# Optimization experiments

Measured on AMD Instinct MI355X. Metric: run time of the kernel, lower is better.

The kernel has to match this reference:

```python
import jax, jax.numpy as jnp
import numpy as np

N_NODES = 100000
N_EDGES = 1_600_000


def _glorot(key, shape):
    fan_in, fan_out = shape
    s = jnp.sqrt(6.0 / (fan_in + fan_out)).astype(jnp.float32)
    return jax.random.uniform(key, shape, jnp.float32, -1.0, 1.0) * s


def setup_inputs() -> dict:
    key = jax.random.key(0)
    ks = jax.random.split(key, 6)
    x = jax.random.normal(ks[0], (N_NODES, 88), jnp.float32)
    edge_index = jax.random.randint(ks[1], (2, N_EDGES), 0, N_NODES, dtype=jnp.int32)
    return {
        "x": x,
        "W1": _glorot(ks[2], (88, 65)), "b1": jnp.zeros((65,), jnp.float32),
        "W2": _glorot(ks[3], (65, 50)), "b2": jnp.zeros((50,), jnp.float32),
        "W3": _glorot(ks[4], (50, 65)), "b3": jnp.zeros((65,), jnp.float32),
        "W4": _glorot(ks[5], (65, 88)), "b4": jnp.zeros((88,), jnp.float32),
        "edge_index": edge_index,
    }


def _gcn_conv(h, W, b, src, dst, norm, n):
    # PyG GCNConv: transform, then normalized neighbor aggregation (self-loops
    # already folded into src/dst/norm).
    h = h @ W                                  # [N, out]
    msg = h[src] * norm[:, None]               # [E+N, out] gather
    return jax.ops.segment_sum(msg, dst, num_segments=n) + b  # scatter-add


def reference(x, W1, b1, W2, b2, W3, b3, W4, b4, edge_index):
    n = x.shape[0]
    loop = jnp.arange(n, dtype=edge_index.dtype)
    src = jnp.concatenate([edge_index[0], loop])   # add self-loops
    dst = jnp.concatenate([edge_index[1], loop])
    deg = jax.ops.segment_sum(jnp.ones_like(dst, dtype=x.dtype), dst, num_segments=n)
    dinv = jnp.where(deg > 0, jax.lax.rsqrt(deg), 0.0)
    norm = dinv[src] * dinv[dst]                   # D^-1/2 (A+I) D^-1/2 edge weights

    # encoder
    h = jax.nn.relu(_gcn_conv(x, W1, b1, src, dst, norm, n))
    h = _gcn_conv(h, W2, b2, src, dst, norm, n)
    # decoder
    h = jax.nn.relu(_gcn_conv(h, W3, b3, src, dst, norm, n))
    return _gcn_conv(h, W4, b4, src, dst, norm, n)
```

## Files before the change

### kernel.cpp

```cpp
#include <hip/hip_runtime.h>

#define BS 256
#define FB 1024
#define NB 256
#define CHUNK 4096
#define CAP 64
#define LCAP 8192
#define GRID_F 1024

using half8 = __attribute__((ext_vector_type(8))) _Float16;

template<typename T>
__device__ __forceinline__ void load8f(const T* p, float (&d)[8]) {
    if constexpr (sizeof(T) == 4) {
        float4 a = *(const float4*)p;
        float4 b = *(const float4*)(p + 4);
        d[0] = a.x; d[1] = a.y; d[2] = a.z; d[3] = a.w;
        d[4] = b.x; d[5] = b.y; d[6] = b.z; d[7] = b.w;
    } else {
        half8 v = *(const half8*)p;
        #pragma unroll
        for (int j = 0; j < 8; ++j) d[j] = (float)v[j];
    }
}
template<typename T>
__device__ __forceinline__ void store8f(T* p, const float (&d)[8]) {
    if constexpr (sizeof(T) == 4) {
        *(float4*)p       = make_float4(d[0], d[1], d[2], d[3]);
        *(float4*)(p + 4) = make_float4(d[4], d[5], d[6], d[7]);
    } else {
        half8 h;
        #pragma unroll
        for (int j = 0; j < 8; ++j) h[j] = (_Float16)d[j];
        *(half8*)p = h;
    }
}


__global__ __launch_bounds__(BS) void k_bucket_g1(
        const int* __restrict__ src, const int* __restrict__ dst,
        unsigned* __restrict__ bbuf, int* __restrict__ bcounts,
        int E, unsigned long long invB, int bsz, int nch,
        const float* __restrict__ x, const float* __restrict__ W1,
        _Float16* __restrict__ hA, int N) {
    constexpr int K = 88, M = 65, LDIN = 88, LDOUT = 72;
    constexpr int CG = 9;
    constexpr int WSTR = K * 8 + 4;
    __shared__ float sh[CG * WSTR];

    if ((int)blockIdx.x < nch) {
        int* lcnt = (int*)sh;
        for (int t = threadIdx.x; t < NB; t += BS) lcnt[t] = 0;
        __syncthreads();
        int base_e = blockIdx.x * CHUNK;
        unsigned* mybuf = bbuf + (size_t)blockIdx.x * NB * CAP;
        #pragma unroll
        for (int j = 0; j < CHUNK / BS; ++j) {
            int e = base_e + j * BS + threadIdx.x;
            if (e < E) {
                int d = dst[e];
                int s = src[e];
                int b = (int)(((unsigned long long)(unsigned)d * invB) >> 40);
                int doff = d - b * bsz;
                int pos = atomicAdd(&lcnt[b], 1);
                if (pos < CAP)
                    mybuf[b * CAP + pos] = ((unsigned)doff << 17) | (unsigned)s;
            }
        }
        __syncthreads();
        for (int t = threadIdx.x; t < NB; t += BS)
            bcounts[blockIdx.x * NB + t] = min(lcnt[t], CAP);
        return;
    }

    float* Wl = sh;
    for (int idx = threadIdx.x; idx < CG * WSTR; idx += BS) {
        int cg = idx / WSTR, rem = idx - cg * WSTR;
        int k = rem >> 3, j = rem & 7;
        int m = cg * 8 + j;
        Wl[idx] = (rem < K * 8 && m < M) ? W1[(size_t)k * M + m] : 0.f;
    }
    __syncthreads();

    int bid = blockIdx.x - nch;
    int nrq = (N + 3) >> 2;
    int idx = bid * BS + threadIdx.x;
    if (idx >= nrq * CG) return;
    int rq = idx / CG;
    int cg = idx - rq * CG;
    int c0 = cg * 8;
    int r0 = rq * 4;
    const float* wb = &Wl[cg * WSTR];

    const float* h[4];
    #pragma unroll
    for (int r = 0; r < 4; ++r) {
        int rr = r0 + r; rr = (rr < N) ? rr : (N - 1);
        h[r] = x + (size_t)rr * LDIN;
    }
    float acc[4][8];
    #pragma unroll
    for (int r = 0; r < 4; ++r)
        #pragma unroll
        for (int m = 0; m < 8; ++m) acc[r][m] = 0.f;

    #pragma unroll 2
    for (int k = 0; k < K; k += 8) {
        float p[4][8];
        load8f(h[0] + k, p[0]);
        load8f(h[1] + k, p[1]);
        load8f(h[2] + k, p[2]);
        load8f(h[3] + k, p[3]);
        const float* wl = wb + k * 8;
        #pragma unroll
        for (int j = 0; j < 8; ++j) {
            float4 wa = *(const float4*)(wl + j * 8);
            float4 wc = *(const float4*)(wl + j * 8 + 4);
            const float wv[8] = {wa.x, wa.y, wa.z, wa.w, wc.x, wc.y, wc.z, wc.w};
            #pragma unroll
            for (int r = 0; r < 4; ++r)
                #pragma unroll
                for (int m = 0; m < 8; ++m)
                    acc[r][m] = fmaf(p[r][j], wv[m], acc[r][m]);
        }
    }
    #pragma unroll
    for (int r = 0; r < 4; ++r) {
        int rr = r0 + r;
        if (rr >= N) break;
        float v[8];
        #pragma unroll
        for (int m = 0; m < 8; ++m) {
            int c = c0 + m;
            v[m] = (c < M) ? acc[r][m] : 0.f;
        }
        store8f(hA + (size_t)rr * LDOUT + c0, v);
    }
}

__global__ __launch_bounds__(FB) void k_cnt(const unsigned* __restrict__ bbuf, const int* __restrict__ bcounts,
                                            int* __restrict__ cnt, int nch, int bsz, int N) {
    __shared__ int lhist[512];
    for (int t = threadIdx.x; t < 512; t += FB) lhist[t] = 0;
    __syncthreads();
    int b = blockIdx.x;
    int lo = b * bsz;
    int total = nch * CAP;
    for (int idx = threadIdx.x; idx < total; idx += FB) {
        int seg = idx >> 6, slot = idx & 63;
        int c = bcounts[seg * NB + b];
        if (slot < c)
            atomicAdd(&lhist[bbuf[((size_t)seg * NB + b) * CAP + slot] >> 17], 1);
    }
    __syncthreads();
    int hi = min(N, lo + bsz);
    for (int t = threadIdx.x; t < hi - lo; t += FB) cnt[lo + t] = lhist[t];
}

__global__ __launch_bounds__(BS) void k_scan1(const int* __restrict__ cnt, int* __restrict__ bsum,
                                              float* __restrict__ dinv, int N) {
    __shared__ int s[BS];
    int i = blockIdx.x * BS + threadIdx.x;
    int v = (i < N) ? cnt[i] : 0;
    if (i < N) dinv[i] = rsqrtf((float)(v + 1));
    s[threadIdx.x] = v;
    __syncthreads();
    for (int off = BS / 2; off > 0; off >>= 1) {
        if (threadIdx.x < off) s[threadIdx.x] += s[threadIdx.x + off];
        __syncthreads();
    }
    if (threadIdx.x == 0) bsum[blockIdx.x] = s[0];
}

__global__ __launch_bounds__(512) void k_scan2(int* bsum, int nb) {
    __shared__ int s[512];
    int t = threadIdx.x;
    int v = (t < nb) ? bsum[t] : 0;
    s[t] = v;
    __syncthreads();
    for (int off = 1; off < 512; off <<= 1) {
        int u = (t >= off) ? s[t - off] : 0;
        __syncthreads();
        s[t] += u;
        __syncthreads();
    }
    if (t < nb) bsum[t] = s[t] - v;
}

__global__ __launch_bounds__(BS) void k_scan3(const int* __restrict__ cnt, const int* __restrict__ boff,
                                              int* __restrict__ row_ptr, int N) {
    __shared__ int s[BS];
    int t = threadIdx.x;
    int i = blockIdx.x * BS + t;
    int v = (i < N) ? cnt[i] : 0;
    s[t] = v;
    __syncthreads();
    for (int off = 1; off < BS; off <<= 1) {
        int u = (t >= off) ? s[t - off] : 0;
        __syncthreads();
        s[t] += u;
        __syncthreads();
    }
    int base = boff[blockIdx.x];
    if (i < N) row_ptr[i] = base + s[t] - v;
    if (i == N - 1) row_ptr[N] = base + s[t];
}

__global__ __launch_bounds__(FB) void k_fill2(const unsigned* __restrict__ bbuf, const int* __restrict__ bcounts,
                                              const int* __restrict__ row_ptr, const float* __restrict__ dinv,
                                              uint2* __restrict__ entries,
                                              int nch, int bsz, int N) {
    __shared__ int cur[512];
    __shared__ float ldinv[512];
    __shared__ unsigned sorted[LCAP];

    int b = blockIdx.x;
    int lo = b * bsz;
    int hi = min(N, lo + bsz);
    int gbase = row_ptr[lo];
    int tot = row_ptr[hi] - gbase;
    for (int t = threadIdx.x; t < hi - lo; t += FB) {
        cur[t] = row_ptr[lo + t] - gbase;
        ldinv[t] = dinv[lo + t];
    }
    __syncthreads();

    int total = nch * CAP;
    for (int idx = threadIdx.x; idx < total; idx += FB) {
        int seg = idx >> 6, slot = idx & 63;
        int c = bcounts[seg * NB + b];
        if (slot < c) {
            unsigned u = bbuf[((size_t)seg * NB + b) * CAP + slot];
            int p = atomicAdd(&cur[u >> 17], 1);
            if (p < LCAP) sorted[p] = u;
        }
    }
    __syncthreads();

    for (int t = threadIdx.x; t < tot; t += FB) {
        unsigned u = sorted[t];
        int s = (int)(u & 0x1FFFFu);
        int doff = (int)(u >> 17);
        float w = dinv[s] * ldinv[doff];
        entries[gbase + t] = make_uint2((unsigned)s, __float_as_uint(w));
    }
}

template<typename TIN, typename TOUT, int M, int M8, int LDI, int LDO, bool BIAS, bool RELU>
__global__ __launch_bounds__(BS) void k_agg(const TIN* __restrict__ T, TOUT* __restrict__ out,
                                            const int* __restrict__ row_ptr, const uint2* __restrict__ entries,
                                            const float* __restrict__ dinv, const float* __restrict__ bias,
                                            int N) {
    constexpr int CG = M8 / 8;
    int idx = blockIdx.x * BS + threadIdx.x;
    if (idx >= N * CG) return;
    int i  = idx / CG;
    int cg = idx - i * CG;
    int c0 = cg * 8;

    float di = dinv[i];
    float w0 = di * di;
    float t0[8];
    load8f(T + (size_t)i * LDI + c0, t0);
    float a0[8], a1[8];
    #pragma unroll
    for (int m = 0; m < 8; ++m) { a0[m] = w0 * t0[m]; a1[m] = 0.f; }

    int e0 = row_ptr[i], e1 = row_ptr[i + 1];
    for (int e = e0; e < e1; e += 8) {
        unsigned sidx[8];
        float w[8];
        #pragma unroll
        for (int j = 0; j < 8; ++j) {
            int ee = e + j;
            int ec = (ee < e1) ? ee : (e1 - 1);
            uint2 u = entries[ec];
            sidx[j] = u.x;
            w[j] = (ee < e1) ? __uint_as_float(u.y) : 0.f;
        }
        #pragma unroll
        for (int j = 0; j < 8; ++j) {
            float g[8];
            load8f(T + (size_t)sidx[j] * LDI + c0, g);
            if (j & 1) {
                #pragma unroll
                for (int m = 0; m < 8; ++m) a1[m] = fmaf(w[j], g[m], a1[m]);
            } else {
                #pragma unroll
                for (int m = 0; m < 8; ++m) a0[m] = fmaf(w[j], g[m], a0[m]);
            }
        }
    }

    #pragma unroll
    for (int m = 0; m < 8; ++m) {
        float v = a0[m] + a1[m];
        if (BIAS && (c0 + m) < M) v += bias[c0 + m];
        if (RELU) v = fmaxf(v, 0.f);
        a0[m] = v;
    }
    store8f(out + (size_t)i * LDO + c0, a0);
}

template<typename TIN, typename TOUT,
         int MA, int MA8, int LDI,
         int MG, int MG8, int LDO,
         int RPB,
         bool ABIAS, bool ARELU, bool GBIAS, bool GRELU>
__global__ __launch_bounds__(BS) void k_agg_gemm(
        const TIN* __restrict__ T, TOUT* __restrict__ out,
        const int* __restrict__ row_ptr, const uint2* __restrict__ entries,
        const float* __restrict__ dinv, const float* __restrict__ Wg,
        const float* __restrict__ ab, const float* __restrict__ gb, int N) {
    static_assert(sizeof(TIN) == 2, "fused kernel expects f16 input rows");
    constexpr int CGA = MA8 / 8;
    constexpr int CGG = MG8 / 8;
    constexpr int K = MA;
    constexpr int WSTR = K * 8 + 4;
    constexpr int BC = 32;

    __shared__ float Wl[CGG * WSTR];
    __shared__ float srow[2][RPB][MA8];

    for (int idx = threadIdx.x; idx < CGG * WSTR; idx += BS) {
        int cg = idx / WSTR, rem = idx - cg * WSTR;
        int k = rem >> 3, j = rem & 7;
        int m = cg * 8 + j;
        Wl[idx] = (rem < K * 8 && m < MG) ? Wg[(size_t)k * MG + m] : 0.f;
    }

    const int t = threadIdx.x;
    const int rA = t / CGA, cgA = t - rA * CGA, c0A = cgA * 8;
    const bool hasA = (rA < RPB);
    const int rB = t / CGG, cgB = t - rB * CGG, c0B = cgB * 8;
    const bool hasB = (rB < RPB);
    const float* wbB = &Wl[cgB * WSTR];
    const int ntiles = (N + RPB - 1) / RPB;

    for (int s = 0; ; ++s) {
        int tA = (int)blockIdx.x + s * (int)gridDim.x;
        int tB = (int)blockIdx.x + (s - 1) * (int)gridDim.x;
        bool anyA = (tA < ntiles);
        bool anyB = (s >= 1) && (tB < ntiles);
        if (!anyA && !anyB) break;
        int bufA = s & 1, bufB = bufA ^ 1;

        int iA = tA * RPB + rA;
        bool doA = anyA && hasA && (iA < N);
        int iB = tB * RPB + rB;
        bool doB = anyB && hasB && (iB < N);

        float bacc[8];
        #pragma unroll
        for (int m = 0; m < 8; ++m) bacc[m] = 0.f;
        int bk = 0;
        const float* hrow = &srow[bufB][hasB ? rB : 0][0];

        if (doA) {
            float di = dinv[iA];
            float w0 = di * di;
            float t0[8];
            load8f(T + (size_t)iA * LDI + c0A, t0);
            float a0[8], a1[8];
            #pragma unroll
            for (int m = 0; m < 8; ++m) { a0[m] = w0 * t0[m]; a1[m] = 0.f; }

            int e0 = row_ptr[iA], e1 = row_ptr[iA + 1];
            for (int e = e0; e < e1; e += 8) {
                unsigned sidx[8];
                float w[8];
                #pragma unroll
                for (int j = 0; j < 8; ++j) {
                    int ee = e + j;
                    int ec = (ee < e1) ? ee : (e1 - 1);
                    uint2 u = entries[ec];
                    sidx[j] = u.x;
                    w[j] = (ee < e1) ? __uint_as_float(u.y) : 0.f;
                }
                half8 g[8];
                #pragma unroll
                for (int j = 0; j < 8; ++j)
                    g[j] = *(const half8*)(T + (size_t)sidx[j] * LDI + c0A);
                if (doB) {
                    int lim = bk + BC; if (lim > K) lim = K;
                    for (; bk < lim; ++bk) {
                        float hv = hrow[bk];
                        const float* wl = wbB + bk * 8;
                        float4 wa = *(const float4*)wl;
                        float4 wc = *(const float4*)(wl + 4);
                        bacc[0] = fmaf(hv, wa.x, bacc[0]);
                        bacc[1] = fmaf(hv, wa.y, bacc[1]);
                        bacc[2] = fmaf(hv, wa.z, bacc[2]);
                        bacc[3] = fmaf(hv, wa.w, bacc[3]);
                        bacc[4] = fmaf(hv, wc.x, bacc[4]);
                        bacc[5] = fmaf(hv, wc.y, bacc[5]);
                        bacc[6] = fmaf(hv, wc.z, bacc[6]);
                        bacc[7] = fmaf(hv, wc.w, bacc[7]);
                    }
                }
                #pragma unroll
                for (int j = 0; j < 8; ++j) {
                    if (j & 1) {
                        #pragma unroll
                        for (int m = 0; m < 8; ++m) a1[m] = fmaf(w[j], (float)g[j][m], a1[m]);
                    } else {
                        #pragma unroll
                        for (int m = 0; m < 8; ++m) a0[m] = fmaf(w[j], (float)g[j][m], a0[m]);
                    }
                }
            }
            #pragma unroll
            for (int m = 0; m < 8; ++m) {
                float v = a0[m] + a1[m];
                if (ABIAS && (c0A + m) < MA) v += ab[c0A + m];
                if (ARELU) v = fmaxf(v, 0.f);
                srow[bufA][rA][c0A + m] = v;
            }
        }
        if (doB) {
            for (; bk < K; ++bk) {
                float hv = hrow[bk];
                const float* wl = wbB + bk * 8;
                float4 wa = *(const float4*)wl;
                float4 wc = *(const float4*)(wl + 4);
                bacc[0] = fmaf(hv, wa.x, bacc[0]);
                bacc[1] = fmaf(hv, wa.y, bacc[1]);
                bacc[2] = fmaf(hv, wa.z, bacc[2]);
                bacc[3] = fmaf(hv, wa.w, bacc[3]);
                bacc[4] = fmaf(hv, wc.x, bacc[4]);
                bacc[5] = fmaf(hv, wc.y, bacc[5]);
                bacc[6] = fmaf(hv, wc.z, bacc[6]);
                bacc[7] = fmaf(hv, wc.w, bacc[7]);
            }
            float v[8];
            #pragma unroll
            for (int m = 0; m < 8; ++m) {
                int c = c0B + m;
                bool in = (c < MG);
                float xv = in ? bacc[m] : 0.f;
                if (GBIAS && in) xv += gb[c];
                if (GRELU) xv = fmaxf(xv, 0.f);
                v[m] = xv;
            }
            store8f(out + (size_t)iB * LDO + c0B, v);
        }
        __syncthreads();
    }
}


extern "C" void kernel_launch(void* const* d_in, const int* in_sizes, int n_in,
                              void* d_out, int out_size, void* d_ws, size_t ws_size,
                              hipStream_t stream) {
    const float* x  = (const float*)d_in[0];
    const float* W1 = (const float*)d_in[1];
    const float* b1 = (const float*)d_in[2];
    const float* W2 = (const float*)d_in[3];
    const float* b2 = (const float*)d_in[4];
    const float* W3 = (const float*)d_in[5];
    const float* b3 = (const float*)d_in[6];
    const float* W4 = (const float*)d_in[7];
    const float* b4 = (const float*)d_in[8];
    const int* edge_index = (const int*)d_in[9];

    const int N = in_sizes[0] / 88;
    const int E = in_sizes[9] / 2;
    const int* src = edge_index;
    const int* dst = edge_index + E;

    const int nch = (E + CHUNK - 1) / CHUNK;
    const int bsz = (N + NB - 1) / NB;
    const unsigned long long invB = ((1ull << 40) + bsz - 1) / bsz;

    auto al = [](size_t b) { return (b + 255) & ~(size_t)255; };
    char* p = (char*)d_ws;
    auto carve = [&](size_t bytes) { void* r = p; p += (bytes + 255) & ~(size_t)255; return r; };
    int*   cnt     = (int*)  carve((size_t)N * 4);
    float* dinv    = (float*)carve((size_t)N * 4);
    int*   row_ptr = (int*)  carve((size_t)(N + 1) * 4);
    int*   bsum    = (int*)  carve(4096);
    uint2* entries = (uint2*)carve((size_t)E * 8);
    _Float16* hA   = (_Float16*)carve((size_t)N * 72 * 2);

    char* ub = p;
    int*      bcounts = (int*)ub;
    unsigned* bbuf    = (unsigned*)(ub + al((size_t)nch * NB * 4));
    size_t csr_bytes  = al((size_t)nch * NB * 4) + al((size_t)nch * NB * CAP * 4);

    size_t hbytes = al((size_t)N * 72 * 2);
    _Float16* hC = (_Float16*)ub;
    _Float16* hD = (_Float16*)(ub + hbytes);
    size_t h_bytes_tot = 2 * hbytes;

    p = ub + (csr_bytes > h_bytes_tot ? csr_bytes : h_bytes_tot);
    (void)p; (void)ws_size;

    int gN = (N + BS - 1) / BS;
    int g1b = (((N + 3) / 4) * 9 + BS - 1) / BS;

    k_bucket_g1<<<nch + g1b, BS, 0, stream>>>(src, dst, bbuf, bcounts, E, invB, bsz, nch,
                                              x, W1, hA, N);
    k_cnt   <<<NB, FB, 0, stream>>>(bbuf, bcounts, cnt, nch, bsz, N);
    k_scan1 <<<gN, BS, 0, stream>>>(cnt, bsum, dinv, N);
    k_scan2 <<<1, 512, 0, stream>>>(bsum, gN);
    k_scan3 <<<gN, BS, 0, stream>>>(cnt, bsum, row_ptr, N);
    k_fill2 <<<NB, FB, 0, stream>>>(bbuf, bcounts, row_ptr, dinv, entries, nch, bsz, N);

    auto agg_grid = [&](int CG) { return (N * CG + BS - 1) / BS; };

    k_agg_gemm<_Float16, _Float16, 65, 72, 72, 50, 56, 56, 28, true, true, false, false>
        <<<GRID_F, BS, 0, stream>>>(hA, hC, row_ptr, entries, dinv, W2, b1, nullptr, N);
    k_agg<_Float16, _Float16, 50, 56, 56, 56, true, false>
        <<<agg_grid(7), BS, 0, stream>>>(hC, hD, row_ptr, entries, dinv, b2, N);
    k_agg_gemm<_Float16, _Float16, 50, 56, 56, 65, 72, 72, 28, false, false, true, true>
        <<<GRID_F, BS, 0, stream>>>(hD, hA, row_ptr, entries, dinv, W3, nullptr, b3, N);
    k_agg_gemm<_Float16, float, 65, 72, 72, 88, 88, 88, 23, false, false, true, false>
        <<<GRID_F, BS, 0, stream>>>(hA, (float*)d_out, row_ptr, entries, dinv, W4, nullptr, b4, N);
}
```

Before: 422.8 us.

## Split fused agg-gemm block into dedicated gather and GEMM warp roles

The fused aggregation+GEMM kernel now runs gather and GEMM in separate warps. The first three waves (192 threads) do the sparse neighbour gather for tile s, and the last wave computes the dense GEMM for tile s-1 out of shared memory. Before, every thread interleaved both jobs. Rows per block and grid sizes are retuned so the gather role fits in 192 threads. The gain is warp specialisation with less register pressure per path, at the cost of a single GEMM wave per block that may become the bottleneck.

```diff
diff --git a/kernel.cpp b/kernel.cpp
--- a/kernel.cpp
+++ b/kernel.cpp
@@ -6,7 +6,6 @@
 #define CHUNK 4096
 #define CAP 64
 #define LCAP 8192
-#define GRID_F 1024
 
 using half8 = __attribute__((ext_vector_type(8))) _Float16;
 
@@ -317,7 +316,8 @@
     constexpr int CGG = MG8 / 8;
     constexpr int K = MA;
     constexpr int WSTR = K * 8 + 4;
-    constexpr int BC = 32;
+    constexpr int AW = 192;
+    static_assert(RPB * CGA <= AW, "gather role must fit 3 waves");
 
     __shared__ float Wl[CGG * WSTR];
     __shared__ float srow[2][RPB][MA8];
@@ -330,11 +330,9 @@
     }
 
     const int t = threadIdx.x;
+    const bool isA = (t < AW);
     const int rA = t / CGA, cgA = t - rA * CGA, c0A = cgA * 8;
-    const bool hasA = (rA < RPB);
-    const int rB = t / CGG, cgB = t - rB * CGG, c0B = cgB * 8;
-    const bool hasB = (rB < RPB);
-    const float* wbB = &Wl[cgB * WSTR];
+    const bool hasA = isA && (rA < RPB);
     const int ntiles = (N + RPB - 1) / RPB;
 
     for (int s = 0; ; ++s) {
@@ -345,104 +343,90 @@
         if (!anyA && !anyB) break;
         int bufA = s & 1, bufB = bufA ^ 1;
 
-        int iA = tA * RPB + rA;
-        bool doA = anyA && hasA && (iA < N);
-        int iB = tB * RPB + rB;
-        bool doB = anyB && hasB && (iB < N);
-
-        float bacc[8];
-        #pragma unroll
-        for (int m = 0; m < 8; ++m) bacc[m] = 0.f;
-        int bk = 0;
-        const float* hrow = &srow[bufB][hasB ? rB : 0][0];
-
-        if (doA) {
-            float di = dinv[iA];
-            float w0 = di * di;
-            float t0[8];
-            load8f(T + (size_t)iA * LDI + c0A, t0);
-            float a0[8], a1[8];
-            #pragma unroll
-            for (int m = 0; m < 8; ++m) { a0[m] = w0 * t0[m]; a1[m] = 0.f; }
-
-            int e0 = row_ptr[iA], e1 = row_ptr[iA + 1];
-            for (int e = e0; e < e1; e += 8) {
-                unsigned sidx[8];
-                float w[8];
-                #pragma unroll
-                for (int j = 0; j < 8; ++j) {
-                    int ee = e + j;
-                    int ec = (ee < e1) ? ee : (e1 - 1);
-                    uint2 u = entries[ec];
-                    sidx[j] = u.x;
-                    w[j] = (ee < e1) ? __uint_as_float(u.y) : 0.f;
-                }
-                half8 g[8];
-                #pragma unroll
-                for (int j = 0; j < 8; ++j)
-                    g[j] = *(const half8*)(T + (size_t)sidx[j] * LDI + c0A);
-                if (doB) {
-                    int lim = bk + BC; if (lim > K) lim = K;
-                    for (; bk < lim; ++bk) {
-                        float hv = hrow[bk];
-                        const float* wl = wbB + bk * 8;
-                        float4 wa = *(const float4*)wl;
-                        float4 wc = *(const float4*)(wl + 4);
-                        bacc[0] = fmaf(hv, wa.x, bacc[0]);
-                        bacc[1] = fmaf(hv, wa.y, bacc[1]);
-                        bacc[2] = fmaf(hv, wa.z, bacc[2]);
-                        bacc[3] = fmaf(hv, wa.w, bacc[3]);
-                        bacc[4] = fmaf(hv, wc.x, bacc[4]);
-                        bacc[5] = fmaf(hv, wc.y, bacc[5]);
-                        bacc[6] = fmaf(hv, wc.z, bacc[6]);
-                        bacc[7] = fmaf(hv, wc.w, bacc[7]);
+        if (hasA && anyA) {
+            int iA = tA * RPB + rA;
+            if (iA < N) {
+                float di = dinv[iA];
+                float w0 = di * di;
+                float t0[8];
+                load8f(T + (size_t)iA * LDI + c0A, t0);
+                float a0[8], a1[8];
+                #pragma unroll
+                for (int m = 0; m < 8; ++m) { a0[m] = w0 * t0[m]; a1[m] = 0.f; }
+
+                int e0 = row_ptr[iA], e1 = row_ptr[iA + 1];
+                for (int e = e0; e < e1; e += 8) {
+                    unsigned sidx[8];
+                    float w[8];
+                    #pragma unroll
+                    for (int j = 0; j < 8; ++j) {
+                        int ee = e + j;
+                        int ec = (ee < e1) ? ee : (e1 - 1);
+                        uint2 u = entries[ec];
+                        sidx[j] = u.x;
+                        w[j] = (ee < e1) ? __uint_as_float(u.y) : 0.f;
+                    }
+                    half8 g[8];
+                    #pragma unroll
+                    for (int j = 0; j < 8; ++j)
+                        g[j] = *(const half8*)(T + (size_t)sidx[j] * LDI + c0A);
+                    #pragma unroll
+                    for (int j = 0; j < 8; ++j) {
+                        if (j & 1) {
+                            #pragma unroll
+                            for (int m = 0; m < 8; ++m) a1[m] = fmaf(w[j], (float)g[j][m], a1[m]);
+                        } else {
+                            #pragma unroll
+                            for (int m = 0; m < 8; ++m) a0[m] = fmaf(w[j], (float)g[j][m], a0[m]);
+                        }
                     }
                 }
                 #pragma unroll
-                for (int j = 0; j < 8; ++j) {
-                    if (j & 1) {
-                        #pragma unroll
-                        for (int m = 0; m < 8; ++m) a1[m] = fmaf(w[j], (float)g[j][m], a1[m]);
-                    } else {
-                        #pragma unroll
-                        for (int m = 0; m < 8; ++m) a0[m] = fmaf(w[j], (float)g[j][m], a0[m]);
-                    }
+                for (int m = 0; m < 8; ++m) {
+                    float v = a0[m] + a1[m];
+                    if (ABIAS && (c0A + m) < MA) v += ab[c0A + m];
+                    if (ARELU) v = fmaxf(v, 0.f);
+                    srow[bufA][rA][c0A + m] = v;
                 }
             }
-            #pragma unroll
-            for (int m = 0; m < 8; ++m) {
-                float v = a0[m] + a1[m];
-                if (ABIAS && (c0A + m) < MA) v += ab[c0A + m];
-                if (ARELU) v = fmaxf(v, 0.f);
-                srow[bufA][rA][c0A + m] = v;
+        } else if (!isA && anyB) {
+            for (int ow = t - AW; ow < RPB * CGG; ow += BS - AW) {
+                int orow = ow / CGG;
+                int ocg  = ow - orow * CGG;
+                int iB = tB * RPB + orow;
+                if (iB >= N) continue;
+                const float* hrow = &srow[bufB][orow][0];
+                const float* wb = &Wl[ocg * WSTR];
+                float bacc[8];
+                #pragma unroll
+                for (int m = 0; m < 8; ++m) bacc[m] = 0.f;
+                #pragma unroll 4
+                for (int k = 0; k < K; ++k) {
+                    float hv = hrow[k];
+                    const float* wl = wb + k * 8;
+                    float4 wa = *(const float4*)wl;
+                    float4 wc = *(const float4*)(wl + 4);
+                    bacc[0] = fmaf(hv, wa.x, bacc[0]);
+                    bacc[1] = fmaf(hv, wa.y, bacc[1]);
+                    bacc[2] = fmaf(hv, wa.z, bacc[2]);
+                    bacc[3] = fmaf(hv, wa.w, bacc[3]);
+                    bacc[4] = fmaf(hv, wc.x, bacc[4]);
+                    bacc[5] = fmaf(hv, wc.y, bacc[5]);
+                    bacc[6] = fmaf(hv, wc.z, bacc[6]);
+                    bacc[7] = fmaf(hv, wc.w, bacc[7]);
+                }
+                float v[8];
+                #pragma unroll
+                for (int m = 0; m < 8; ++m) {
+                    int c = ocg * 8 + m;
+                    bool in = (c < MG);
+                    float xv = in ? bacc[m] : 0.f;
+                    if (GBIAS && in) xv += gb[c];
+                    if (GRELU) xv = fmaxf(xv, 0.f);
+                    v[m] = xv;
+                }
+                store8f(out + (size_t)iB * LDO + ocg * 8, v);
             }
-        }
-        if (doB) {
-            for (; bk < K; ++bk) {
-                float hv = hrow[bk];
-                const float* wl = wbB + bk * 8;
-                float4 wa = *(const float4*)wl;
-                float4 wc = *(const float4*)(wl + 4);
-                bacc[0] = fmaf(hv, wa.x, bacc[0]);
-                bacc[1] = fmaf(hv, wa.y, bacc[1]);
-                bacc[2] = fmaf(hv, wa.z, bacc[2]);
-                bacc[3] = fmaf(hv, wa.w, bacc[3]);
-                bacc[4] = fmaf(hv, wc.x, bacc[4]);
-                bacc[5] = fmaf(hv, wc.y, bacc[5]);
-                bacc[6] = fmaf(hv, wc.z, bacc[6]);
-                bacc[7] = fmaf(hv, wc.w, bacc[7]);
-            }
-            float v[8];
-            #pragma unroll
-            for (int m = 0; m < 8; ++m) {
-                int c = c0B + m;
-                bool in = (c < MG);
-                float xv = in ? bacc[m] : 0.f;
-                if (GBIAS && in) xv += gb[c];
-                if (GRELU) xv = fmaxf(xv, 0.f);
-                v[m] = xv;
-            }
-            store8f(out + (size_t)iB * LDO + c0B, v);
         }
         __syncthreads();
     }
@@ -508,12 +492,12 @@
 
     auto agg_grid = [&](int CG) { return (N * CG + BS - 1) / BS; };
 
-    k_agg_gemm<_Float16, _Float16, 65, 72, 72, 50, 56, 56, 28, true, true, false, false>
-        <<<GRID_F, BS, 0, stream>>>(hA, hC, row_ptr, entries, dinv, W2, b1, nullptr, N);
+    k_agg_gemm<_Float16, _Float16, 65, 72, 72, 50, 56, 56, 21, true, true, false, false>
+        <<<1536, BS, 0, stream>>>(hA, hC, row_ptr, entries, dinv, W2, b1, nullptr, N);
     k_agg<_Float16, _Float16, 50, 56, 56, 56, true, false>
         <<<agg_grid(7), BS, 0, stream>>>(hC, hD, row_ptr, entries, dinv, b2, N);
-    k_agg_gemm<_Float16, _Float16, 50, 56, 56, 65, 72, 72, 28, false, false, true, true>
-        <<<GRID_F, BS, 0, stream>>>(hD, hA, row_ptr, entries, dinv, W3, nullptr, b3, N);
-    k_agg_gemm<_Float16, float, 65, 72, 72, 88, 88, 88, 23, false, false, true, false>
-        <<<GRID_F, BS, 0, stream>>>(hA, (float*)d_out, row_ptr, entries, dinv, W4, nullptr, b4, N);
-}
+    k_agg_gemm<_Float16, _Float16, 50, 56, 56, 65, 72, 72, 27, false, false, true, true>
+        <<<1536, BS, 0, stream>>>(hD, hA, row_ptr, entries, dinv, W3, nullptr, b3, N);
+    k_agg_gemm<_Float16, float, 65, 72, 72, 88, 88, 88, 21, false, false, true, false>
+        <<<1024, BS, 0, stream>>>(hA, (float*)d_out, row_ptr, entries, dinv, W4, nullptr, b4, N);
+}
```

After: 537.0 us. 27.0% more time.
